# Kernel tuning notes

Measured on AMD Instinct MI355X. Metric: run time of the kernel, lower is better.

The kernel has to match this reference:

```python
import jax, jax.numpy as jnp
import numpy as np

B, T, V, E, H, M, U, W = 8, 64, 30000, 256, 512, 512, 32, 512


def setup_inputs():
    rng = np.random.RandomState(0)
    ks = jax.random.split(jax.random.key(0), 20)
    u_len = rng.randint(U // 2, U + 1, size=B).astype(np.int32)
    w_len = rng.randint(W // 2, W + 1, size=B).astype(np.int32)
    # word2utt[b, j] = utterance index owning word j; padded words -> last valid utt
    w2u = np.zeros((B, W), np.int32)
    for b in range(B):
        j = np.minimum(np.arange(W), w_len[b] - 1)
        w2u[b] = np.minimum((j * u_len[b]) // w_len[b], u_len[b] - 1)
    s = 0.02
    p = lambda i, shp: jax.random.normal(ks[i], shp, jnp.float32) * s
    emb = p(0, (V, E)).at[0].set(0.0)  # padding_idx=0
    return {
        'target': jax.random.randint(ks[1], (B, T), 0, V, jnp.int32),
        'u_output': jax.random.normal(ks[2], (B, U, M), jnp.float32),
        'w_output': jax.random.normal(ks[3], (B, W, M), jnp.float32),
        'u_len': jnp.asarray(u_len), 'w_len': jnp.asarray(w_len), 'word2utt': jnp.asarray(w2u),
        'emb': emb,
        'W_ih': p(4, (3 * H, E)), 'W_hh': p(5, (3 * H, H)),
        'b_ih': p(6, (3 * H,)), 'b_hh': p(7, (3 * H,)),
        'Wu': p(8, (H, M)), 'bu': p(9, (H,)),
        'Ww': p(10, (H, M)), 'bw': p(11, (H,)),
        'Wo': p(12, (V, H + M)), 'bo': p(13, (V,)),
        'Wd': p(14, (1, V)), 'Wy': p(15, (1, E)),
        'Ws': p(16, (1, H)), 'bs': p(17, (1,)),
    }


def reference(target, u_output, w_output, u_len, w_len, word2utt,
              emb, W_ih, W_hh, b_ih, b_hh, Wu, bu, Ww, bw, Wo, bo, Wd, Wy, Ws, bs):
    Bn = target.shape[0]
    Un = u_output.shape[1]
    Vn = Wo.shape[0]
    Au = jnp.einsum('bum,hm->buh', u_output, Wu) + bu  # attention_u(u_output)
    Aw = jnp.einsum('bwm,hm->bwh', w_output, Ww) + bw  # attention_w(w_output)
    u_mask = jnp.arange(Un)[None, :] < u_len[:, None]               # [B,U]
    w_mask = jnp.arange(w_output.shape[1])[None, :] < w_len[:, None]  # [B,W]
    # initial hidden = last valid utterance state (mem_hidden == dec_hidden)
    h0 = jnp.take_along_axis(u_output, (u_len - 1)[:, None, None], axis=1)[:, 0, :]

    def gru_step(x, h):
        gi = x @ W_ih.T + b_ih
        gh = h @ W_hh.T + b_hh
        ir, iz, inn = jnp.split(gi, 3, axis=-1)
        hr, hz, hn = jnp.split(gh, 3, axis=-1)
        r = jax.nn.sigmoid(ir + hr)
        z = jax.nn.sigmoid(iz + hz)
        n = jnp.tanh(inn + r * hn)
        return (1.0 - z) * n + z * h

    def seg_softmax(sw, seg, valid):  # per-batch ragged per-utterance softmax over words
        swm = jnp.where(valid, sw, -jnp.inf)
        m = jax.ops.segment_max(swm, seg, num_segments=Un)
        e = jnp.where(valid, jnp.exp(sw - m[seg]), 0.0)
        d = jax.ops.segment_sum(e, seg, num_segments=Un)
        return e / d[seg]

    def step(carry, yt):
        h, d_prev, eu_prev = carry
        y = emb[yt]                               # [B,E]
        h_new = gru_step(y, h)                    # rnn_output == new hidden (1 layer)
        su = jnp.einsum('bh,buh->bu', h_new, Au)
        su = jax.nn.softmax(jnp.where(u_mask, su, -jnp.inf), axis=-1)
        gamma = jax.nn.sigmoid(d_prev @ Wd.T + y @ Wy.T + h_new @ Ws.T + bs)  # [B,1]
        su = (1.0 - gamma) * su + gamma * eu_prev
        su = su / jnp.sum(su, axis=-1, keepdims=True)
        sw = jnp.einsum('bh,bwh->bw', h_new, Aw)
        pw = jax.vmap(seg_softmax)(sw, word2utt, w_mask)        # [B,W]
        suw = jnp.take_along_axis(su, word2utt, axis=1) * pw    # [B,W]
        ctx = jnp.einsum('bw,bwm->bm', suw, w_output)
        logits = jnp.concatenate([ctx, h_new], axis=-1) @ Wo.T + bo
        dt = jax.nn.log_softmax(logits, axis=-1)
        return (h_new, dt, su), (dt, suw, su)

    init = (h0, jnp.zeros((Bn, Vn), jnp.float32), jnp.zeros((Bn, Un), jnp.float32))
    _, (dts, suws, sus) = jax.lax.scan(step, init, target.T)
    dec_output = jnp.swapaxes(dts, 0, 1)   # [B,T,V]
    scores_uw = jnp.swapaxes(suws, 0, 1)   # [B,T,W]
    scores_u = jnp.swapaxes(sus, 0, 1)     # [B,T,U]
    return dec_output, scores_uw, scores_u
```

## Files before the change

kernel.cpp:

```cpp
#include <hip/hip_runtime.h>
#include <math.h>

typedef unsigned short ushort_t;
typedef unsigned int uint_t;
typedef unsigned long long ulong_t;
typedef __attribute__((ext_vector_type(8))) short s16x8;
typedef __attribute__((ext_vector_type(4))) float f32x4;

#define BB 8
#define TT 64
#define VV 30000
#define VP 30080
#define EE 256
#define HH 512
#define MM 512
#define UU 32
#define WW 512
#define G3 1536
#define NDB 235
#define NBG 64

#define OFF_GI    0
#define OFF_YALL  786432
#define OFF_WY    917504
#define OFF_H0    918016
#define OFF_HALL  922112
#define OFF_HU    1184256
#define OFF_HW    1446400
#define OFF_HS    1708544
#define OFF_HWV   1709056
#define OFF_P     1709568
#define OFF_SW    1725952
#define OFF_C     1988096
#define OFF_E     6182400
#define OFF_WV    6198784
#define OFF_PART  6200320
#define OFF_LSE   6208512
#define OFF_WOV   6209024
#define OFF_HBT   13909504
#define OFF_SYNC  14040576

#define DEC_SZ (BB*TT*VV)
#define SUW_OFF DEC_SZ
#define SU_OFF  (DEC_SZ + BB*TT*WW)

__device__ __forceinline__ float sigm(float x){ return 1.0f/(1.0f+__expf(-x)); }
__device__ __forceinline__ ushort_t to_bf16(float f){
  uint_t u = __float_as_uint(f);
  return (ushort_t)((u + 0x7fffu + ((u>>16)&1u)) >> 16);
}


template<int TRANSB>
__global__ void __launch_bounds__(256)
k_gemm_b(const float* __restrict__ A, int lda, int aS,
         const float* __restrict__ B, int ldb, int bS,
         const float* __restrict__ bias,
         float* __restrict__ C, int ldc, int cS, int K){
  A += (size_t)blockIdx.z * aS;
  B += (size_t)blockIdx.z * bS;
  C += (size_t)blockIdx.z * cS;
  __shared__ float As[32][65];
  __shared__ float Bs[32][65];
  int tid = threadIdx.x;
  int bx = blockIdx.x, by = blockIdx.y;
  int tx = tid & 15, ty = tid >> 4;
  float acc[4][4] = {};
  for (int k0 = 0; k0 < K; k0 += 32){
    {
      int r = tid >> 2, cbase = (tid & 3) * 8;
      const float* ap = A + (size_t)(by*64 + r)*lda + k0 + cbase;
      #pragma unroll
      for (int i=0;i<8;++i) As[cbase+i][r] = ap[i];
    }
    if (TRANSB){
      int r = tid >> 2, cbase = (tid & 3) * 8;
      const float* bp = B + (size_t)(bx*64 + r)*ldb + k0 + cbase;
      #pragma unroll
      for (int i=0;i<8;++i) Bs[cbase+i][r] = bp[i];
    } else {
      int kk = tid >> 3, cbase = (tid & 7) * 8;
      const float* bp = B + (size_t)(k0 + kk)*ldb + bx*64 + cbase;
      #pragma unroll
      for (int i=0;i<8;++i) Bs[kk][cbase+i] = bp[i];
    }
    __syncthreads();
    #pragma unroll
    for (int kk=0;kk<32;++kk){
      float a0=As[kk][ty*4+0], a1=As[kk][ty*4+1], a2=As[kk][ty*4+2], a3=As[kk][ty*4+3];
      float b0=Bs[kk][tx*4+0], b1=Bs[kk][tx*4+1], b2=Bs[kk][tx*4+2], b3=Bs[kk][tx*4+3];
      acc[0][0]+=a0*b0; acc[0][1]+=a0*b1; acc[0][2]+=a0*b2; acc[0][3]+=a0*b3;
      acc[1][0]+=a1*b0; acc[1][1]+=a1*b1; acc[1][2]+=a1*b2; acc[1][3]+=a1*b3;
      acc[2][0]+=a2*b0; acc[2][1]+=a2*b1; acc[2][2]+=a2*b2; acc[2][3]+=a2*b3;
      acc[3][0]+=a3*b0; acc[3][1]+=a3*b1; acc[3][2]+=a3*b2; acc[3][3]+=a3*b3;
    }
    __syncthreads();
  }
  #pragma unroll
  for (int i=0;i<4;++i){
    int row = by*64 + ty*4 + i;
    #pragma unroll
    for (int j=0;j<4;++j){
      int col = bx*64 + tx*4 + j;
      float v = acc[i][j];
      if (bias) v += bias[col];
      C[(size_t)row*ldc + col] = v;
    }
  }
}

__global__ void k_y(const int* __restrict__ target, const float* __restrict__ emb,
                    const float* __restrict__ Wy, float* __restrict__ ws){
  int bt = blockIdx.x;
  int e = threadIdx.x;
  __shared__ float r[256];
  int tok = target[bt];
  float v = emb[tok*EE + e];
  ws[OFF_YALL + bt*EE + e] = v;
  r[e] = v * Wy[e];
  __syncthreads();
  for (int s=128; s; s>>=1){ if (e<s) r[e]+=r[e+s]; __syncthreads(); }
  if (e == 0) ws[OFF_WY + bt] = r[0];
}

__global__ void k_h0(const float* __restrict__ u_output, const int* __restrict__ u_len,
                     float* __restrict__ ws){
  int idx = blockIdx.x*256 + threadIdx.x;
  int b = idx >> 9; int k = idx & 511;
  int u = u_len[b]-1;
  ws[OFF_H0 + idx] = u_output[(b*UU+u)*MM + k];
}

__global__ void __launch_bounds__(256)
k_wovc(const float* __restrict__ Wo, ushort_t* __restrict__ wov){
  int idx8 = blockIdx.x*256 + threadIdx.x;
  int v = idx8 >> 6;
  int k8 = (idx8 & 63) << 3;
  uint_t u0=0,u1=0,u2=0,u3=0;
  if (v < VV){
    const float* src = Wo + (size_t)v*1024 + k8;
    float4 f0 = *(const float4*)src;
    float4 f1 = *(const float4*)(src+4);
    u0 = (uint_t)to_bf16(f0.x) | ((uint_t)to_bf16(f0.y) << 16);
    u1 = (uint_t)to_bf16(f0.z) | ((uint_t)to_bf16(f0.w) << 16);
    u2 = (uint_t)to_bf16(f1.x) | ((uint_t)to_bf16(f1.y) << 16);
    u3 = (uint_t)to_bf16(f1.z) | ((uint_t)to_bf16(f1.w) << 16);
  }
  uint4 pk = make_uint4(u0,u1,u2,u3);
  *(uint4*)(wov + (size_t)idx8*8) = pk;
}

__global__ void __launch_bounds__(256)
k_wv(const float* __restrict__ Wo, const float* __restrict__ bo,
     const float* __restrict__ Wd, float* __restrict__ wv){
  __shared__ float wds[128];
  __shared__ float red[256];
  int tid = threadIdx.x;
  int v0 = blockIdx.x*128;
  float pbo=0.f, pwd=0.f;
  if (tid < 128){
    int v = v0 + tid;
    float wd = (v<VV)? Wd[v] : 0.f;
    wds[tid] = wd;
    pbo = wd * ((v<VV)? bo[v] : 0.f);
    pwd = wd;
  }
  __syncthreads();
  float4 acc = {0,0,0,0};
  int nmax = (v0 + 128 <= VV) ? 128 : (VV - v0);
  for (int i=0;i<nmax;++i){
    float wd = wds[i];
    float4 w4 = *(const float4*)(Wo + (size_t)(v0+i)*1024 + tid*4);
    acc.x += wd*w4.x; acc.y += wd*w4.y; acc.z += wd*w4.z; acc.w += wd*w4.w;
  }
  atomicAdd(&wv[tid*4+0], acc.x);
  atomicAdd(&wv[tid*4+1], acc.y);
  atomicAdd(&wv[tid*4+2], acc.z);
  atomicAdd(&wv[tid*4+3], acc.w);
  red[tid] = pbo; __syncthreads();
  for (int s=128; s; s>>=1){ if (tid<s) red[tid]+=red[tid+s]; __syncthreads(); }
  if (tid==0) atomicAdd(&wv[1024], red[0]);
  __syncthreads();
  red[tid] = pwd; __syncthreads();
  for (int s=128; s; s>>=1){ if (tid<s) red[tid]+=red[tid+s]; __syncthreads(); }
  if (tid==0) atomicAdd(&wv[1025], red[0]);
}


__global__ void __launch_bounds__(1024)
k_gru_persist(const float* __restrict__ W_hh, const float* __restrict__ b_hh,
              float* __restrict__ ws){
  uint_t* flags = (uint_t*)(ws + OFF_SYNC);
  int tid  = threadIdx.x;
  int wid  = tid >> 6;
  int lane = tid & 63;
  int half = wid >> 3;
  int kl   = wid & 7;
  int k    = blockIdx.x*8 + kl;
  const float* gi_all = ws + OFF_GI;
  const float* wr = W_hh + (size_t)k*HH;
  const float* wz = W_hh + (size_t)(HH+k)*HH;
  const float* wn = W_hh + (size_t)(2*HH+k)*HH;
  __shared__ float red[16][24];

  for (int t=0; t<TT; ++t){
    const float* hin = (t==0) ? (ws+OFF_H0) : (ws+OFF_HALL + (size_t)(t-1)*4096);
    float* hout = ws + OFF_HALL + (size_t)t*4096;
    float pr[8], pz[8], pn[8];
    #pragma unroll
    for (int b=0;b<8;++b){ pr[b]=0.f; pz[b]=0.f; pn[b]=0.f; }
    int kk0 = half*256 + lane;
    #pragma unroll
    for (int it=0; it<4; ++it){
      int kk = kk0 + it*64;
      float w1 = wr[kk], w2 = wz[kk], w3 = wn[kk];
      #pragma unroll
      for (int b=0;b<8;++b){
        float hv = hin[b*HH+kk];
        pr[b] += hv*w1; pz[b] += hv*w2; pn[b] += hv*w3;
      }
    }
    #pragma unroll
    for (int off=32; off; off>>=1){
      #pragma unroll
      for (int b=0;b<8;++b){
        pr[b] += __shfl_xor(pr[b],off);
        pz[b] += __shfl_xor(pz[b],off);
        pn[b] += __shfl_xor(pn[b],off);
      }
    }
    if (lane == 0){
      #pragma unroll
      for (int b=0;b<8;++b){
        red[wid][b]    = pr[b];
        red[wid][8+b]  = pz[b];
        red[wid][16+b] = pn[b];
      }
    }
    __syncthreads();
    if (tid < 64){
      int klx = tid >> 3, b = tid & 7;
      int k2 = blockIdx.x*8 + klx;
      float prs = red[klx][b]    + red[8+klx][b];
      float pzs = red[klx][8+b]  + red[8+klx][8+b];
      float pns = red[klx][16+b] + red[8+klx][16+b];
      const float* gi = gi_all + (b*TT + t)*G3;
      float r = sigm(gi[k2]      + prs + b_hh[k2]);
      float z = sigm(gi[HH+k2]   + pzs + b_hh[HH+k2]);
      float n = tanhf(gi[2*HH+k2] + r*(pns + b_hh[2*HH+k2]));
      hout[b*HH+k2] = (1.f-z)*n + z*hin[b*HH+k2];
    }
    __syncthreads();
    if (tid == 0)
      __hip_atomic_store(&flags[blockIdx.x*32], (uint_t)(t+1), __ATOMIC_RELEASE, __HIP_MEMORY_SCOPE_AGENT);
    if (tid < NBG){
      while (__hip_atomic_load(&flags[tid*32], __ATOMIC_RELAXED, __HIP_MEMORY_SCOPE_AGENT) < (uint_t)(t+1))
        __builtin_amdgcn_s_sleep(1);
    }
    __syncthreads();
  }
  {
    ushort_t* hbt = (ushort_t*)(ws + OFF_HBT);
    int base = (blockIdx.x*1024 + tid)*4;
    #pragma unroll
    for (int i=0;i<4;++i) hbt[base+i] = to_bf16(ws[OFF_HALL + base + i]);
  }
}


__global__ void __launch_bounds__(256)
k_lh_mfma(const float* __restrict__ Wo, const float* __restrict__ bo,
          const ushort_t* __restrict__ hbt, float* __restrict__ out){
  int tid = threadIdx.x;
  int wv = tid >> 6, l = tid & 63;
  int lm = l & 15, lg = l >> 4;
  int vbase = blockIdx.x*128 + wv*32;
  int rbase = blockIdx.y*128;
  f32x4 acc[2][8];
  #pragma unroll
  for (int s=0;s<2;++s)
    #pragma unroll
    for (int rt=0;rt<8;++rt) acc[s][rt] = (f32x4){0.f,0.f,0.f,0.f};

  for (int k0 = 0; k0 < 512; k0 += 32){
    int kk = k0 + lg*8;
    union { uint_t u[4]; s16x8 s; } af[2];
    #pragma unroll
    for (int s=0;s<2;++s){
      int v = vbase + s*16 + lm; if (v >= VV) v = VV-1;
      const float* ap = Wo + (size_t)v*1024 + 512 + kk;
      float4 f0 = *(const float4*)ap;
      float4 f1 = *(const float4*)(ap+4);
      af[s].u[0] = ((__float_as_uint(f0.x)+0x8000u)>>16) | ((__float_as_uint(f0.y)+0x8000u) & 0xffff0000u);
      af[s].u[1] = ((__float_as_uint(f0.z)+0x8000u)>>16) | ((__float_as_uint(f0.w)+0x8000u) & 0xffff0000u);
      af[s].u[2] = ((__float_as_uint(f1.x)+0x8000u)>>16) | ((__float_as_uint(f1.y)+0x8000u) & 0xffff0000u);
      af[s].u[3] = ((__float_as_uint(f1.z)+0x8000u)>>16) | ((__float_as_uint(f1.w)+0x8000u) & 0xffff0000u);
    }
    #pragma unroll
    for (int rt=0;rt<8;++rt){
      const ushort_t* bp = hbt + (size_t)(rbase + rt*16 + lm)*HH + kk;
      s16x8 bf = *(const s16x8*)bp;
      acc[0][rt] = __builtin_amdgcn_mfma_f32_16x16x32_bf16(af[0].s, bf, acc[0][rt], 0, 0, 0);
      acc[1][rt] = __builtin_amdgcn_mfma_f32_16x16x32_bf16(af[1].s, bf, acc[1][rt], 0, 0, 0);
    }
  }
  float bv[2][4];
  #pragma unroll
  for (int s=0;s<2;++s)
    #pragma unroll
    for (int r=0;r<4;++r){
      int v = vbase + s*16 + lg*4 + r;
      bv[s][r] = (v < VV) ? bo[v] : 0.f;
    }
  #pragma unroll
  for (int rt=0;rt<8;++rt){
    int row = rbase + rt*16 + lm;
    float* orow = out + (size_t)((row&7)*TT + (row>>3))*VV;
    #pragma unroll
    for (int s=0;s<2;++s){
      #pragma unroll
      for (int r=0;r<4;++r){
        int v = vbase + s*16 + lg*4 + r;
        if (v < VV) orow[v] = acc[s][rt][r] + bv[s][r];
      }
    }
  }
}


__global__ void k_hdots(const float* __restrict__ Ws, float* __restrict__ ws){
  int wid  = blockIdx.x*4 + (threadIdx.x>>6);
  int lane = threadIdx.x & 63;
  int row = wid >> 1, which = wid & 1;
  const float* h = ws + OFF_HALL + row*HH;
  const float* src = which ? (ws + OFF_WV + 512) : Ws;
  float acc = 0.f;
  for (int k=lane; k<HH; k+=64) acc += h[k]*src[k];
  for (int off=32; off; off>>=1) acc += __shfl_xor(acc, off);
  if (lane == 0) (which ? ws+OFF_HWV : ws+OFF_HS)[row] = acc;
}

__global__ void k_p(const float* __restrict__ u_output, const int* __restrict__ u_len,
                    float* __restrict__ ws){
  int row = blockIdx.x;
  int b = row & 7;
  int tid = threadIdx.x;
  __shared__ float su_s[UU];
  {
    int u = tid >> 3, l8 = tid & 7;
    const float* hu = ws + OFF_HU + row*512;
    const float* uo = u_output + (size_t)(b*UU + u)*MM;
    float acc = 0.f;
    for (int m=l8; m<MM; m+=8) acc += hu[m]*uo[m];
    acc += __shfl_xor(acc,1); acc += __shfl_xor(acc,2); acc += __shfl_xor(acc,4);
    if (l8 == 0) su_s[u] = acc;
  }
  __syncthreads();
  if (tid < 32){
    int ul = u_len[b];
    float sv = su_s[tid];
    bool valid = tid < ul;
    float mv = valid ? sv : -1e30f;
    for (int off=16; off; off>>=1) mv = fmaxf(mv, __shfl_xor(mv, off));
    float e = valid ? __expf(sv - mv) : 0.f;
    float ssum = e;
    for (int off=16; off; off>>=1) ssum += __shfl_xor(ssum, off);
    ws[OFF_P + row*UU + tid] = e/ssum;
  }
}

__global__ void k_pw(const int* __restrict__ word2utt, const int* __restrict__ w_len,
                     float* __restrict__ ws){
  int row = blockIdx.x;
  int b = row & 7;
  int tid = threadIdx.x;
  __shared__ float sarr[WW];
  __shared__ int   seg[WW];
  __shared__ float marr[UU], darr[UU];
  int wl = w_len[b];
  float* swrow = ws + OFF_SW + row*WW;
  for (int w=tid; w<WW; w+=256){ sarr[w] = swrow[w]; seg[w] = word2utt[b*WW+w]; }
  __syncthreads();
  {
    int g = tid>>3, l8 = tid&7;
    float mv = -1e30f;
    for (int w=l8; w<wl; w+=8) if (seg[w]==g) mv = fmaxf(mv, sarr[w]);
    mv = fmaxf(mv, __shfl_xor(mv,1)); mv = fmaxf(mv, __shfl_xor(mv,2)); mv = fmaxf(mv, __shfl_xor(mv,4));
    float d = 0.f;
    for (int w=l8; w<wl; w+=8) if (seg[w]==g) d += __expf(sarr[w]-mv);
    d += __shfl_xor(d,1); d += __shfl_xor(d,2); d += __shfl_xor(d,4);
    if (l8 == 0){ marr[g]=mv; darr[g]=d; }
  }
  __syncthreads();
  for (int w=tid; w<WW; w+=256){
    float val = 0.f;
    if (w < wl){ int u = seg[w]; val = __expf(sarr[w]-marr[u])/darr[u]; }
    swrow[w] = val;
  }
}

__global__ void __launch_bounds__(256)
k_C(const float* __restrict__ w_output, const int* __restrict__ w_len,
    const int* __restrict__ u_len, const int* __restrict__ word2utt,
    float* __restrict__ ws){
  int row = blockIdx.x;
  int b = row & 7;
  int tid = threadIdx.x;
  __shared__ float pws[WW];
  __shared__ int   seg[WW];
  __shared__ int   st[UU], en[UU];
  __shared__ float wvs[512];
  __shared__ float red32[UU][4];
  int wl = w_len[b], ul = u_len[b];
  const float* pwrow = ws + OFF_SW + row*WW;
  for (int w=tid; w<WW; w+=256){ pws[w] = pwrow[w]; seg[w] = word2utt[b*WW+w]; }
  for (int m=tid; m<512; m+=256) wvs[m] = ws[OFF_WV + m];
  if (tid < UU){ st[tid]=0; en[tid]=0; }
  __syncthreads();
  for (int w=tid; w<wl; w+=256){
    int s = seg[w];
    if (w==0 || seg[w-1]!=s) st[s]=w;
    if (w==wl-1 || seg[w+1]!=s) en[s]=w+1;
  }
  __syncthreads();
  ushort_t* Cu = (ushort_t*)(ws + OFF_C);
  int m0 = tid, m1 = tid + 256;
  int lane = tid & 63, wvi = tid >> 6;
  for (int u=0; u<UU; ++u){
    float acc0=0.f, acc1=0.f;
    if (u < ul){
      int s = st[u], e = en[u];
      for (int w=s; w<e; ++w){
        float p = pws[w];
        const float* wo = w_output + ((size_t)(b*WW+w))*MM;
        acc0 += p*wo[m0];
        acc1 += p*wo[m1];
      }
    }
    size_t cbase = ((size_t)row*UU + u)*512;
    Cu[cbase + m0] = to_bf16(acc0);
    Cu[cbase + m1] = to_bf16(acc1);
    float part = acc0*wvs[m0] + acc1*wvs[m1];
    #pragma unroll
    for (int off=32; off; off>>=1) part += __shfl_xor(part, off);
    if (lane == 0) red32[u][wvi] = part;
  }
  __syncthreads();
  if (tid < UU)
    ws[OFF_E + row*UU + tid] = red32[tid][0]+red32[tid][1]+red32[tid][2]+red32[tid][3];
}


__global__ void __launch_bounds__(512)
k_decode_persist(const int* __restrict__ u_len, const float* __restrict__ bs,
                 const ushort_t* __restrict__ wov,
                 float* __restrict__ ws, float* __restrict__ out){
  int bid = blockIdx.x;
  int tid = threadIdx.x;
  uint_t* sy     = (uint_t*)(ws + OFF_SYNC);
  uint_t* flags  = sy + 8192;
  uint_t* flags2 = sy + 16000;
  __shared__ float suL[8][32];
  __shared__ float qbufL[8], lseL[8], gamL[8];
  __shared__ int   ulS[8];
  __shared__ uint_t cbU[16*260];
  __shared__ float2 wred[8][8];
  __shared__ float smr[256], ssr[256];
  __shared__ float cst[4];
  if (tid == 0){ cst[0]=bs[0]; cst[1]=ws[OFF_WV+1024]; cst[2]=ws[OFF_WV+1025]; }
  if (tid < 8){ qbufL[tid]=0.f; lseL[tid]=0.f; ulS[tid]=u_len[tid]; }
  if (tid < 256) suL[tid>>5][tid&31] = 0.f;
  for (int i=tid; i<8*260; i+=512) cbU[8*260 + i] = 0u;
  __syncthreads();

  int wid = tid >> 6, l = tid & 63;
  int lm = l & 15, lgp = l >> 4;

  for (int t=0; t<TT; ++t){
    if (t > 0 && tid < 8)
      lseL[tid] = __hip_atomic_load((const float*)(ws + OFF_LSE + (t-1)*8 + tid),
                                    __ATOMIC_RELAXED, __HIP_MEMORY_SCOPE_AGENT);
    __syncthreads();
    if (tid < 8){
      float pd = 0.f;
      if (t > 0)
        pd = qbufL[tid] + ws[OFF_HWV + (t-1)*8 + tid] + cst[1] - lseL[tid]*cst[2];
      gamL[tid] = sigm(pd + ws[OFF_WY + tid*TT + t] + ws[OFF_HS + t*8 + tid] + cst[0]);
    }
    __syncthreads();
    if (tid < 256){
      int b = tid >> 5, j = tid & 31;
      int row = t*8 + b;
      float gg = gamL[b];
      float p = ws[OFF_P + row*UU + j];
      float eu = suL[b][j];
      float mix = (1.f-gg)*p + gg*eu;
      float s2 = mix;
      #pragma unroll
      for (int off=16; off; off>>=1) s2 += __shfl_xor(s2, off);
      float su = mix / s2;
      suL[b][j] = su;
      float qp = su * ws[OFF_E + row*UU + j];
      #pragma unroll
      for (int off=16; off; off>>=1) qp += __shfl_xor(qp, off);
      if (j == 0) qbufL[b] = qp;
    }
    __syncthreads();
    if (bid < 8 && tid < 32)
      out[SU_OFF + (bid*TT + t)*UU + tid] = suL[bid][tid];
    {
      int b = tid >> 6, l64 = tid & 63;
      int m8 = l64 * 8;
      int row = t*8 + b;
      int ul = ulS[b];
      const ushort_t* Crow = (const ushort_t*)(ws + OFF_C) + ((size_t)row*UU)*512 + m8;
      float acc[8];
      #pragma unroll
      for (int i=0;i<8;++i) acc[i]=0.f;
      for (int u=0; u<ul; ++u){
        float su = suL[b][u];
        uint4 c0 = *(const uint4*)(Crow + (size_t)u*512);
        uint_t cc[4] = {c0.x,c0.y,c0.z,c0.w};
        #pragma unroll
        for (int q=0;q<4;++q){
          acc[2*q]   += su * __uint_as_float((cc[q] & 0xffffu) << 16);
          acc[2*q+1] += su * __uint_as_float((cc[q] >> 16) << 16);
        }
      }
      #pragma unroll
      for (int q=0;q<4;++q){
        uint_t pk = (uint_t)to_bf16(acc[2*q]) | ((uint_t)to_bf16(acc[2*q+1]) << 16);
        cbU[b*260 + l64*4 + q] = pk;
      }
    }
    __syncthreads();

    {
      int vbase = bid*128 + wid*16;
      f32x4 acc0 = {0.f,0.f,0.f,0.f};
      const ushort_t* ap0 = wov + (size_t)(vbase + lm)*512 + lgp*8;
      const uint_t* cbrow = cbU + lm*260 + lgp*4;
      #pragma unroll
      for (int ks=0; ks<16; ++ks){
        s16x8 av0 = *(const s16x8*)(ap0 + ks*32);
        s16x8 bv  = *(const s16x8*)(cbrow + ks*16);
        acc0 = __builtin_amdgcn_mfma_f32_16x16x32_bf16(av0, bv, acc0, 0, 0, 0);
      }
      float pm = -1e30f, ps = 0.f;
      if (lm < 8){
        float* orow = out + ((size_t)(lm*TT + t))*VV;
        int vb = vbase + lgp*4;
        float l4v[4];
        if (vb + 3 < VV){
          float4 o = *(const float4*)(orow + vb);
          float g0 = acc0[0]+o.x, g1 = acc0[1]+o.y, g2 = acc0[2]+o.z, g3 = acc0[3]+o.w;
          *(float4*)(orow + vb) = make_float4(g0,g1,g2,g3);
          l4v[0]=g0; l4v[1]=g1; l4v[2]=g2; l4v[3]=g3;
        } else {
          #pragma unroll
          for (int r=0;r<4;++r){
            int v = vb + r;
            float g = -1e30f;
            if (v < VV){ g = acc0[r] + orow[v]; orow[v] = g; }
            l4v[r] = g;
          }
        }
        #pragma unroll
        for (int i=0;i<4;++i) pm = fmaxf(pm, l4v[i]);
        #pragma unroll
        for (int i=0;i<4;++i) ps += (l4v[i] > -5e29f) ? __expf(l4v[i]-pm) : 0.f;
      }
      #pragma unroll
      for (int off=16; off<=32; off<<=1){
        float mo = __shfl_xor(pm, off);
        float so = __shfl_xor(ps, off);
        float nm = fmaxf(pm, mo);
        ps = ps*__expf(pm-nm) + so*__expf(mo-nm);
        pm = nm;
      }
      if (lgp == 0 && lm < 8) wred[wid][lm] = make_float2(pm, ps);
    }
    __syncthreads();
    if (tid < 8){
      float m = -1e30f, s = 0.f;
      #pragma unroll
      for (int w=0; w<8; ++w){
        float2 e = wred[w][tid];
        float nm = fmaxf(m, e.x);
        s = s*__expf(m-nm) + e.y*__expf(e.x-nm);
        m = nm;
      }
      *(float2*)(ws + OFF_PART + (t&1)*4096 + (bid*8 + tid)*2) = make_float2(m, s);
    }

    __syncthreads();
    if (tid == 0)
      __hip_atomic_store(&flags[bid*32], (uint_t)(t+1), __ATOMIC_RELEASE, __HIP_MEMORY_SCOPE_AGENT);
    if (bid < 8){
      if (tid < NDB){
        while (__hip_atomic_load(&flags[tid*32], __ATOMIC_RELAXED, __HIP_MEMORY_SCOPE_AGENT) < (uint_t)(t+1))
          __builtin_amdgcn_s_sleep(2);
      }
      __syncthreads();
      {
        const ulong_t* partq = (const ulong_t*)(ws + OFF_PART + (t&1)*4096);
        float m = -1e30f, s = 0.f;
        if (tid < NDB){
          ulong_t pq = __hip_atomic_load(&partq[tid*8 + bid], __ATOMIC_RELAXED, __HIP_MEMORY_SCOPE_AGENT);
          m = __uint_as_float((uint_t)pq);
          s = __uint_as_float((uint_t)(pq >> 32));
        }
        if (tid < 256){ smr[tid]=m; ssr[tid]=s; }
        __syncthreads();
        for (int st=128; st; st>>=1){
          if (tid < st){
            float m1 = smr[tid], s1 = ssr[tid];
            float m2 = smr[tid+st], s2 = ssr[tid+st];
            float mm = fmaxf(m1, m2);
            ssr[tid] = s1*__expf(m1-mm) + s2*__expf(m2-mm);
            smr[tid] = mm;
          }
          __syncthreads();
        }
        if (tid == 0){
          __hip_atomic_store((float*)(ws + OFF_LSE + t*8 + bid), smr[0] + logf(ssr[0]),
                             __ATOMIC_RELAXED, __HIP_MEMORY_SCOPE_AGENT);
          __hip_atomic_store(&flags2[bid*32], (uint_t)(t+1), __ATOMIC_RELEASE, __HIP_MEMORY_SCOPE_AGENT);
        }
      }
    }
    if (tid < 8){
      while (__hip_atomic_load(&flags2[tid*32], __ATOMIC_RELAXED, __HIP_MEMORY_SCOPE_AGENT) < (uint_t)(t+1))
        __builtin_amdgcn_s_sleep(1);
    }
    __syncthreads();
  }
}


__global__ void k_sub2(const float* __restrict__ ws, float* __restrict__ out){
  int v = blockIdx.x*256 + threadIdx.x;
  int tb = blockIdx.y;
  int t = tb >> 3, b = tb & 7;
  if (v < VV) out[(size_t)(b*TT+t)*VV + v] -= ws[OFF_LSE + tb];
}

__global__ void k_suw2(const int* __restrict__ word2utt, const float* __restrict__ ws,
                       float* __restrict__ out){
  int row = blockIdx.x;
  int t = row >> 3, b = row & 7;
  int tid = threadIdx.x;
  for (int w=tid; w<WW; w+=256){
    int seg = word2utt[b*WW + w];
    float su = out[SU_OFF + (b*TT+t)*UU + seg];
    float pw = ws[OFF_SW + row*WW + w];
    out[SUW_OFF + (b*TT+t)*WW + w] = su*pw;
  }
}

extern "C" void kernel_launch(void* const* d_in, const int* in_sizes, int n_in,
                              void* d_out, int out_size, void* d_ws, size_t ws_size,
                              hipStream_t stream) {
  const int*   target   = (const int*)d_in[0];
  const float* u_output = (const float*)d_in[1];
  const float* w_output = (const float*)d_in[2];
  const int*   u_len    = (const int*)d_in[3];
  const int*   w_len    = (const int*)d_in[4];
  const int*   word2utt = (const int*)d_in[5];
  const float* emb      = (const float*)d_in[6];
  const float* W_ih     = (const float*)d_in[7];
  const float* W_hh     = (const float*)d_in[8];
  const float* b_ih     = (const float*)d_in[9];
  const float* b_hh     = (const float*)d_in[10];
  const float* Wu       = (const float*)d_in[11];
  const float* Ww       = (const float*)d_in[13];
  const float* Wo       = (const float*)d_in[15];
  const float* bo       = (const float*)d_in[16];
  const float* Wd       = (const float*)d_in[17];
  const float* Wy       = (const float*)d_in[18];
  const float* Ws       = (const float*)d_in[19];
  const float* bs       = (const float*)d_in[20];
  float* out = (float*)d_out;
  float* ws  = (float*)d_ws;
  ushort_t* wov = (ushort_t*)(ws + OFF_WOV);
  ushort_t* hbt = (ushort_t*)(ws + OFF_HBT);

  hipMemsetAsync(ws + OFF_SYNC, 0, 16384*sizeof(float), stream);

  hipLaunchKernelGGL(k_y, dim3(512), dim3(256), 0, stream, target, emb, Wy, ws);
  hipLaunchKernelGGL((k_gemm_b<1>), dim3(24,8,1), dim3(256), 0, stream,
                     ws+OFF_YALL, 256, 0, W_ih, 256, 0, b_ih, ws+OFF_GI, 1536, 0, 256);
  hipLaunchKernelGGL(k_h0, dim3(16), dim3(256), 0, stream, u_output, u_len, ws);
  hipLaunchKernelGGL(k_wovc, dim3(7520), dim3(256), 0, stream, Wo, wov);
  hipMemsetAsync(ws + OFF_WV, 0, 1536*sizeof(float), stream);
  hipLaunchKernelGGL(k_wv, dim3(235), dim3(256), 0, stream, Wo, bo, Wd, ws+OFF_WV);

  hipLaunchKernelGGL(k_gru_persist, dim3(NBG), dim3(1024), 0, stream, W_hh, b_hh, ws);

  hipLaunchKernelGGL(k_lh_mfma, dim3(235, 4), dim3(256), 0, stream, Wo, bo, hbt, out);
  hipLaunchKernelGGL((k_gemm_b<0>), dim3(8,8,1), dim3(256), 0, stream,
                     ws+OFF_HALL, 512, 0, Wu, 512, 0, (const float*)nullptr, ws+OFF_HU, 512, 0, 512);
  hipLaunchKernelGGL((k_gemm_b<0>), dim3(8,8,1), dim3(256), 0, stream,
                     ws+OFF_HALL, 512, 0, Ww, 512, 0, (const float*)nullptr, ws+OFF_HW, 512, 0, 512);
  hipLaunchKernelGGL(k_hdots, dim3(256), dim3(256), 0, stream, Ws, ws);
  hipLaunchKernelGGL(k_p, dim3(512), dim3(256), 0, stream, u_output, u_len, ws);
  hipLaunchKernelGGL((k_gemm_b<1>), dim3(8,1,8), dim3(256), 0, stream,
                     ws+OFF_HW, 4096, 512, w_output, 512, 262144, (const float*)nullptr,
                     ws+OFF_SW, 4096, 512, 512);
  hipLaunchKernelGGL(k_pw, dim3(512), dim3(256), 0, stream, word2utt, w_len, ws);
  hipLaunchKernelGGL(k_C, dim3(512), dim3(256), 0, stream,
                     w_output, w_len, u_len, word2utt, ws);

  hipLaunchKernelGGL(k_decode_persist, dim3(NDB), dim3(512), 0, stream,
                     u_len, bs, wov, ws, out);

  hipLaunchKernelGGL(k_sub2, dim3(118, 512), dim3(256), 0, stream, ws, out);
  hipLaunchKernelGGL(k_suw2, dim3(512), dim3(256), 0, stream, word2utt, ws, out);
}
```

Before: 1.929 ms.

## Split context logits linearly, prefetch next step's GEMM, add dedicated LSE reducer block

The mixed attention su is (1-g)*p + g*eu, normalised. The context logits are therefore split algebraically into two parts: a P-weighted context term precomputed in k_C, and an eu-weighted term. Each is multiplied by Wo through MFMA for the next timestep before that step's gamma is known. A separate extra block now does the log-sum-exp reduction and signals a single go flag, so the decode blocks no longer run the serial 8-block reduction followed by an all-wait. This is meant to take the C-weighted sum and the MFMA off the critical path between steps. The cost is a doubled MFMA count, an extra workspace buffer, and a persistent block that busy-waits on the flags.

```diff
diff --git a/kernel.cpp b/kernel.cpp
--- a/kernel.cpp
+++ b/kernel.cpp
@@ -39,6 +39,7 @@
 #define OFF_WOV   6209024
 #define OFF_HBT   13909504
 #define OFF_SYNC  14040576
+#define OFF_PC    14056960
 
 #define DEC_SZ (BB*TT*VV)
 #define SUW_OFF DEC_SZ
@@ -410,12 +411,13 @@
   __shared__ int   seg[WW];
   __shared__ int   st[UU], en[UU];
   __shared__ float wvs[512];
+  __shared__ float parr[UU];
   __shared__ float red32[UU][4];
   int wl = w_len[b], ul = u_len[b];
   const float* pwrow = ws + OFF_SW + row*WW;
   for (int w=tid; w<WW; w+=256){ pws[w] = pwrow[w]; seg[w] = word2utt[b*WW+w]; }
   for (int m=tid; m<512; m+=256) wvs[m] = ws[OFF_WV + m];
-  if (tid < UU){ st[tid]=0; en[tid]=0; }
+  if (tid < UU){ st[tid]=0; en[tid]=0; parr[tid] = ws[OFF_P + row*UU + tid]; }
   __syncthreads();
   for (int w=tid; w<wl; w+=256){
     int s = seg[w];
@@ -426,6 +428,7 @@
   ushort_t* Cu = (ushort_t*)(ws + OFF_C);
   int m0 = tid, m1 = tid + 256;
   int lane = tid & 63, wvi = tid >> 6;
+  float pc0 = 0.f, pc1 = 0.f;
   for (int u=0; u<UU; ++u){
     float acc0=0.f, acc1=0.f;
     if (u < ul){
@@ -440,11 +443,15 @@
     size_t cbase = ((size_t)row*UU + u)*512;
     Cu[cbase + m0] = to_bf16(acc0);
     Cu[cbase + m1] = to_bf16(acc1);
+    float pu = parr[u];
+    pc0 += pu*acc0; pc1 += pu*acc1;
     float part = acc0*wvs[m0] + acc1*wvs[m1];
     #pragma unroll
     for (int off=32; off; off>>=1) part += __shfl_xor(part, off);
     if (lane == 0) red32[u][wvi] = part;
   }
+  ws[OFF_PC + (size_t)row*512 + m0] = pc0;
+  ws[OFF_PC + (size_t)row*512 + m1] = pc1;
   __syncthreads();
   if (tid < UU)
     ws[OFF_E + row*UU + tid] = red32[tid][0]+red32[tid][1]+red32[tid][2]+red32[tid][3];
@@ -457,29 +464,111 @@
                  float* __restrict__ ws, float* __restrict__ out){
   int bid = blockIdx.x;
   int tid = threadIdx.x;
-  uint_t* sy     = (uint_t*)(ws + OFF_SYNC);
-  uint_t* flags  = sy + 8192;
-  uint_t* flags2 = sy + 16000;
+  uint_t* sy    = (uint_t*)(ws + OFF_SYNC);
+  uint_t* flags = sy + 8192;
+  uint_t* go    = sy + 16000;
+
+  if (bid == NDB){
+    int wid = tid >> 6, l = tid & 63;
+    for (int t=0; t<TT; ++t){
+      if (tid < NDB){
+        while (__hip_atomic_load(&flags[tid*32], __ATOMIC_RELAXED, __HIP_MEMORY_SCOPE_AGENT) < (uint_t)(t+1))
+          __builtin_amdgcn_s_sleep(1);
+      }
+      __syncthreads();
+      {
+        const ulong_t* partq = (const ulong_t*)(ws + OFF_PART + (t&1)*4096);
+        float ma = -1e30f, sa = 0.f;
+        #pragma unroll
+        for (int it=0; it<4; ++it){
+          int i = l + it*64;
+          if (i < NDB){
+            ulong_t pq = __hip_atomic_load(&partq[i*8 + wid], __ATOMIC_RELAXED, __HIP_MEMORY_SCOPE_AGENT);
+            float m = __uint_as_float((uint_t)pq);
+            float s = __uint_as_float((uint_t)(pq >> 32));
+            float mm = fmaxf(ma, m);
+            sa = sa*__expf(ma-mm) + s*__expf(m-mm);
+            ma = mm;
+          }
+        }
+        #pragma unroll
+        for (int off=32; off; off>>=1){
+          float mo = __shfl_xor(ma, off);
+          float so = __shfl_xor(sa, off);
+          float mm = fmaxf(ma, mo);
+          sa = sa*__expf(ma-mm) + so*__expf(mo-mm);
+          ma = mm;
+        }
+        if (l == 0)
+          __hip_atomic_store((float*)(ws + OFF_LSE + t*8 + wid), ma + logf(sa),
+                             __ATOMIC_RELAXED, __HIP_MEMORY_SCOPE_AGENT);
+      }
+      __syncthreads();
+      if (tid == 0)
+        __hip_atomic_store(go, (uint_t)(t+1), __ATOMIC_RELEASE, __HIP_MEMORY_SCOPE_AGENT);
+    }
+    return;
+  }
+
   __shared__ float suL[8][32];
-  __shared__ float qbufL[8], lseL[8], gamL[8];
+  __shared__ float qbufL[8], lseL[8], gamL[8], s2L[8];
   __shared__ int   ulS[8];
-  __shared__ uint_t cbU[16*260];
+  __shared__ uint_t cbPC[16*260];
+  __shared__ uint_t cbEC[16*260];
   __shared__ float2 wred[8][8];
-  __shared__ float smr[256], ssr[256];
   __shared__ float cst[4];
   if (tid == 0){ cst[0]=bs[0]; cst[1]=ws[OFF_WV+1024]; cst[2]=ws[OFF_WV+1025]; }
-  if (tid < 8){ qbufL[tid]=0.f; lseL[tid]=0.f; ulS[tid]=u_len[tid]; }
+  if (tid < 8){ qbufL[tid]=0.f; lseL[tid]=0.f; s2L[tid]=1.f; ulS[tid]=u_len[tid]; }
   if (tid < 256) suL[tid>>5][tid&31] = 0.f;
-  for (int i=tid; i<8*260; i+=512) cbU[8*260 + i] = 0u;
+  for (int i=tid; i<8*260; i+=512){ cbPC[8*260 + i] = 0u; cbEC[8*260 + i] = 0u; }
   __syncthreads();
 
   int wid = tid >> 6, l = tid & 63;
   int lm = l & 15, lgp = l >> 4;
+  int vbase = bid*128 + wid*16;
+  const ushort_t* ap0 = wov + (size_t)(vbase + lm)*512 + lgp*8;
+  const uint_t* cbrowP = cbPC + lm*260 + lgp*4;
+  const uint_t* cbrowE = cbEC + lm*260 + lgp*4;
+
+  f32x4 LPC = {0.f,0.f,0.f,0.f};
+  f32x4 LEC = {0.f,0.f,0.f,0.f};
+  float Lh4[4] = {0.f,0.f,0.f,0.f};
+
+  {
+    int b = tid >> 6, l64 = tid & 63;
+    const float* PCrow = ws + OFF_PC + (size_t)(b)*512 + l64*8;
+    float4 p0 = *(const float4*)PCrow;
+    float4 p1 = *(const float4*)(PCrow + 4);
+    cbPC[b*260 + l64*4 + 0] = (uint_t)to_bf16(p0.x) | ((uint_t)to_bf16(p0.y) << 16);
+    cbPC[b*260 + l64*4 + 1] = (uint_t)to_bf16(p0.z) | ((uint_t)to_bf16(p0.w) << 16);
+    cbPC[b*260 + l64*4 + 2] = (uint_t)to_bf16(p1.x) | ((uint_t)to_bf16(p1.y) << 16);
+    cbPC[b*260 + l64*4 + 3] = (uint_t)to_bf16(p1.z) | ((uint_t)to_bf16(p1.w) << 16);
+  }
+  __syncthreads();
+  #pragma unroll
+  for (int ks=0; ks<16; ++ks){
+    s16x8 av = *(const s16x8*)(ap0 + ks*32);
+    s16x8 bp = *(const s16x8*)(cbrowP + ks*16);
+    LPC = __builtin_amdgcn_mfma_f32_16x16x32_bf16(av, bp, LPC, 0, 0, 0);
+  }
+  if (lm < 8){
+    const float* orow = out + ((size_t)(lm*TT + 0))*VV;
+    int vb = vbase + lgp*4;
+    #pragma unroll
+    for (int r=0;r<4;++r){ int v = vb + r; Lh4[r] = (v < VV) ? orow[v] : 0.f; }
+  }
 
   for (int t=0; t<TT; ++t){
-    if (t > 0 && tid < 8)
-      lseL[tid] = __hip_atomic_load((const float*)(ws + OFF_LSE + (t-1)*8 + tid),
-                                    __ATOMIC_RELAXED, __HIP_MEMORY_SCOPE_AGENT);
+    if (t > 0){
+      if (tid == 0){
+        while (__hip_atomic_load(go, __ATOMIC_RELAXED, __HIP_MEMORY_SCOPE_AGENT) < (uint_t)t)
+          __builtin_amdgcn_s_sleep(1);
+      }
+      __syncthreads();
+      if (tid < 8)
+        lseL[tid] = __hip_atomic_load((const float*)(ws + OFF_LSE + (t-1)*8 + tid),
+                                      __ATOMIC_RELAXED, __HIP_MEMORY_SCOPE_AGENT);
+    }
     __syncthreads();
     if (tid < 8){
       float pd = 0.f;
@@ -500,6 +589,7 @@
       for (int off=16; off; off>>=1) s2 += __shfl_xor(s2, off);
       float su = mix / s2;
       suL[b][j] = su;
+      if (j == 0) s2L[b] = s2;
       float qp = su * ws[OFF_E + row*UU + j];
       #pragma unroll
       for (int off=16; off; off>>=1) qp += __shfl_xor(qp, off);
@@ -508,61 +598,25 @@
     __syncthreads();
     if (bid < 8 && tid < 32)
       out[SU_OFF + (bid*TT + t)*UU + tid] = suL[bid][tid];
+
     {
-      int b = tid >> 6, l64 = tid & 63;
-      int m8 = l64 * 8;
-      int row = t*8 + b;
-      int ul = ulS[b];
-      const ushort_t* Crow = (const ushort_t*)(ws + OFF_C) + ((size_t)row*UU)*512 + m8;
-      float acc[8];
-      #pragma unroll
-      for (int i=0;i<8;++i) acc[i]=0.f;
-      for (int u=0; u<ul; ++u){
-        float su = suL[b][u];
-        uint4 c0 = *(const uint4*)(Crow + (size_t)u*512);
-        uint_t cc[4] = {c0.x,c0.y,c0.z,c0.w};
-        #pragma unroll
-        for (int q=0;q<4;++q){
-          acc[2*q]   += su * __uint_as_float((cc[q] & 0xffffu) << 16);
-          acc[2*q+1] += su * __uint_as_float((cc[q] >> 16) << 16);
-        }
-      }
-      #pragma unroll
-      for (int q=0;q<4;++q){
-        uint_t pk = (uint_t)to_bf16(acc[2*q]) | ((uint_t)to_bf16(acc[2*q+1]) << 16);
-        cbU[b*260 + l64*4 + q] = pk;
-      }
-    }
-    __syncthreads();
-
-    {
-      int vbase = bid*128 + wid*16;
-      f32x4 acc0 = {0.f,0.f,0.f,0.f};
-      const ushort_t* ap0 = wov + (size_t)(vbase + lm)*512 + lgp*8;
-      const uint_t* cbrow = cbU + lm*260 + lgp*4;
-      #pragma unroll
-      for (int ks=0; ks<16; ++ks){
-        s16x8 av0 = *(const s16x8*)(ap0 + ks*32);
-        s16x8 bv  = *(const s16x8*)(cbrow + ks*16);
-        acc0 = __builtin_amdgcn_mfma_f32_16x16x32_bf16(av0, bv, acc0, 0, 0, 0);
-      }
       float pm = -1e30f, ps = 0.f;
       if (lm < 8){
+        float gg = gamL[lm];
+        float inv = 1.f / s2L[lm];
         float* orow = out + ((size_t)(lm*TT + t))*VV;
         int vb = vbase + lgp*4;
         float l4v[4];
+        #pragma unroll
+        for (int r=0;r<4;++r)
+          l4v[r] = ((1.f-gg)*LPC[r] + gg*LEC[r])*inv + Lh4[r];
         if (vb + 3 < VV){
-          float4 o = *(const float4*)(orow + vb);
-          float g0 = acc0[0]+o.x, g1 = acc0[1]+o.y, g2 = acc0[2]+o.z, g3 = acc0[3]+o.w;
-          *(float4*)(orow + vb) = make_float4(g0,g1,g2,g3);
-          l4v[0]=g0; l4v[1]=g1; l4v[2]=g2; l4v[3]=g3;
+          *(float4*)(orow + vb) = make_float4(l4v[0],l4v[1],l4v[2],l4v[3]);
         } else {
           #pragma unroll
           for (int r=0;r<4;++r){
             int v = vb + r;
-            float g = -1e30f;
-            if (v < VV){ g = acc0[r] + orow[v]; orow[v] = g; }
-            l4v[r] = g;
+            if (v < VV) orow[v] = l4v[r]; else l4v[r] = -1e30f;
           }
         }
         #pragma unroll
@@ -592,48 +646,60 @@
       }
       *(float2*)(ws + OFF_PART + (t&1)*4096 + (bid*8 + tid)*2) = make_float2(m, s);
     }
-
     __syncthreads();
     if (tid == 0)
       __hip_atomic_store(&flags[bid*32], (uint_t)(t+1), __ATOMIC_RELEASE, __HIP_MEMORY_SCOPE_AGENT);
-    if (bid < 8){
-      if (tid < NDB){
-        while (__hip_atomic_load(&flags[tid*32], __ATOMIC_RELAXED, __HIP_MEMORY_SCOPE_AGENT) < (uint_t)(t+1))
-          __builtin_amdgcn_s_sleep(2);
+
+    if (t < TT-1){
+      int tn = t + 1;
+      {
+        int b = tid >> 6, l64 = tid & 63;
+        int m8 = l64 * 8;
+        int row = tn*8 + b;
+        int ul = ulS[b];
+        const ushort_t* Crow = (const ushort_t*)(ws + OFF_C) + ((size_t)row*UU)*512 + m8;
+        float acc[8];
+        #pragma unroll
+        for (int i=0;i<8;++i) acc[i]=0.f;
+        for (int u=0; u<ul; ++u){
+          float su = suL[b][u];
+          uint4 c0 = *(const uint4*)(Crow + (size_t)u*512);
+          uint_t cc[4] = {c0.x,c0.y,c0.z,c0.w};
+          #pragma unroll
+          for (int q=0;q<4;++q){
+            acc[2*q]   += su * __uint_as_float((cc[q] & 0xffffu) << 16);
+            acc[2*q+1] += su * __uint_as_float((cc[q] >> 16) << 16);
+          }
+        }
+        #pragma unroll
+        for (int q=0;q<4;++q)
+          cbEC[b*260 + l64*4 + q] = (uint_t)to_bf16(acc[2*q]) | ((uint_t)to_bf16(acc[2*q+1]) << 16);
+        const float* PCrow = ws + OFF_PC + (size_t)row*512 + m8;
+        float4 p0 = *(const float4*)PCrow;
+        float4 p1 = *(const float4*)(PCrow + 4);
+        cbPC[b*260 + l64*4 + 0] = (uint_t)to_bf16(p0.x) | ((uint_t)to_bf16(p0.y) << 16);
+        cbPC[b*260 + l64*4 + 1] = (uint_t)to_bf16(p0.z) | ((uint_t)to_bf16(p0.w) << 16);
+        cbPC[b*260 + l64*4 + 2] = (uint_t)to_bf16(p1.x) | ((uint_t)to_bf16(p1.y) << 16);
+        cbPC[b*260 + l64*4 + 3] = (uint_t)to_bf16(p1.z) | ((uint_t)to_bf16(p1.w) << 16);
       }
       __syncthreads();
-      {
-        const ulong_t* partq = (const ulong_t*)(ws + OFF_PART + (t&1)*4096);
-        float m = -1e30f, s = 0.f;
-        if (tid < NDB){
-          ulong_t pq = __hip_atomic_load(&partq[tid*8 + bid], __ATOMIC_RELAXED, __HIP_MEMORY_SCOPE_AGENT);
-          m = __uint_as_float((uint_t)pq);
-          s = __uint_as_float((uint_t)(pq >> 32));
-        }
-        if (tid < 256){ smr[tid]=m; ssr[tid]=s; }
-        __syncthreads();
-        for (int st=128; st; st>>=1){
-          if (tid < st){
-            float m1 = smr[tid], s1 = ssr[tid];
-            float m2 = smr[tid+st], s2 = ssr[tid+st];
-            float mm = fmaxf(m1, m2);
-            ssr[tid] = s1*__expf(m1-mm) + s2*__expf(m2-mm);
-            smr[tid] = mm;
-          }
-          __syncthreads();
-        }
-        if (tid == 0){
-          __hip_atomic_store((float*)(ws + OFF_LSE + t*8 + bid), smr[0] + logf(ssr[0]),
-                             __ATOMIC_RELAXED, __HIP_MEMORY_SCOPE_AGENT);
-          __hip_atomic_store(&flags2[bid*32], (uint_t)(t+1), __ATOMIC_RELEASE, __HIP_MEMORY_SCOPE_AGENT);
-        }
-      }
-    }
-    if (tid < 8){
-      while (__hip_atomic_load(&flags2[tid*32], __ATOMIC_RELAXED, __HIP_MEMORY_SCOPE_AGENT) < (uint_t)(t+1))
-        __builtin_amdgcn_s_sleep(1);
-    }
-    __syncthreads();
+      LPC = (f32x4){0.f,0.f,0.f,0.f};
+      LEC = (f32x4){0.f,0.f,0.f,0.f};
+      #pragma unroll
+      for (int ks=0; ks<16; ++ks){
+        s16x8 av = *(const s16x8*)(ap0 + ks*32);
+        s16x8 bp = *(const s16x8*)(cbrowP + ks*16);
+        s16x8 be = *(const s16x8*)(cbrowE + ks*16);
+        LPC = __builtin_amdgcn_mfma_f32_16x16x32_bf16(av, bp, LPC, 0, 0, 0);
+        LEC = __builtin_amdgcn_mfma_f32_16x16x32_bf16(av, be, LEC, 0, 0, 0);
+      }
+      if (lm < 8){
+        const float* orow = out + ((size_t)(lm*TT + tn))*VV;
+        int vb = vbase + lgp*4;
+        #pragma unroll
+        for (int r=0;r<4;++r){ int v = vb + r; Lh4[r] = (v < VV) ? orow[v] : 0.f; }
+      }
+    }
   }
 }
 
@@ -711,7 +777,7 @@
   hipLaunchKernelGGL(k_C, dim3(512), dim3(256), 0, stream,
                      w_output, w_len, u_len, word2utt, ws);
 
-  hipLaunchKernelGGL(k_decode_persist, dim3(NDB), dim3(512), 0, stream,
+  hipLaunchKernelGGL(k_decode_persist, dim3(NDB+1), dim3(512), 0, stream,
                      u_len, bs, wov, ws, out);
 
   hipLaunchKernelGGL(k_sub2, dim3(118, 512), dim3(256), 0, stream, ws, out);
```

After: 1.887 ms, median of 3. 2.2% less time.
